# Optimization experiments

Measured on AMD Instinct MI355X. Metric: run time of the kernel, lower is better.

## Reference

```python
import jax, jax.numpy as jnp
import numpy as np

SELECTED_CLASSES = 5  # selected_classes init arg; loop body is identical each iteration
EPS = 1e-5            # nn.InstanceNorm2d default eps


def setup_inputs() -> dict:
    key = jax.random.key(0)
    k1, k2, k3 = jax.random.split(key, 3)
    x = jax.random.normal(k1, (8, 256, 128, 128), dtype=jnp.float32)
    masks = jax.random.uniform(k2, (8, 512, 512), dtype=jnp.float32)
    conv_w = jax.random.normal(k3, (1, 3, 7, 7), dtype=jnp.float32) * 0.05  # CFR_branches[0], no bias
    in_gamma = jnp.ones((256,), dtype=jnp.float32)   # InstanceNorm2d affine weight
    in_beta = jnp.zeros((256,), dtype=jnp.float32)   # InstanceNorm2d affine bias
    return {"x": x, "masks": masks, "conv_w": conv_w, "in_gamma": in_gamma, "in_beta": in_beta}


def reference(x, masks, conv_w, in_gamma, in_beta):
    B, C, H, W = x.shape
    m = masks[:, None, :, :] if masks.ndim == 3 else masks  # [B,1,Hm,Wm]
    # F.interpolate(..., size=(H,H), mode='bilinear', align_corners=False) -> half-pixel bilinear
    m = jax.image.resize(m, (B, 1, H, H), method="bilinear")
    mid = x * m                                             # [B,C,H,W]
    avg_out = jnp.mean(mid, axis=1, keepdims=True)          # [B,1,H,W]
    max_out = jnp.max(mid, axis=1, keepdims=True)           # [B,1,H,W]
    atten = jnp.concatenate([avg_out, max_out, m], axis=1)  # [B,3,H,W]
    atten = jax.lax.conv_general_dilated(
        atten, conv_w, window_strides=(1, 1), padding=[(3, 3), (3, 3)],
        dimension_numbers=("NCHW", "OIHW", "NCHW"))        # [B,1,H,W]
    atten = jax.nn.sigmoid(atten)
    out = mid * atten
    # set_class_mask_matrix: kmeans1d is not imported -> except branch -> all-ones mask;
    # Regional_Normalization therefore reduces to InstanceNorm2d(out).
    mu = jnp.mean(out, axis=(2, 3), keepdims=True)
    var = jnp.var(out, axis=(2, 3), keepdims=True)
    rn = (out - mu) * jax.lax.rsqrt(var + EPS)
    rn = rn * in_gamma[None, :, None, None] + in_beta[None, :, None, None]
    # loop over selected_classes produces identical outs (idx stays 0); sum == scale
    return jax.nn.relu(SELECTED_CLASSES * rn)
```

## Files before the change

### kernel.cpp

```cpp
#include <hip/hip_runtime.h>
#include <math.h>

#define BB 8
#define CC 256
#define HH 128
#define WW 128
#define HWP 16384
#define MH 512
#define MW 512
#define NPIX (BB*HWP)
#define IQ 4096

__global__ __launch_bounds__(256) void k1(const float* __restrict__ masks,
                                          const float* __restrict__ x,
                                          float* __restrict__ m_out,
                                          float* __restrict__ cs,
                                          float* __restrict__ cm) {
    int bid = blockIdx.x, tid = threadIdx.x;
    if ((bid & 1) == 0) {
        int t = (bid >> 1) * 256 + tid;
        int j = t & 127, i = (t >> 7) & 127, b = t >> 14;
        const float Wt[8] = {1.f, 3.f, 5.f, 7.f, 7.f, 5.f, 3.f, 1.f};
        const float* mb = masks + (size_t)b * (MH * MW);
        int r0 = 4 * i - 2, c0 = 4 * j - 2;
        float cwgt[8];
        int ccl[8];
        float sh = 0.f;
        #pragma unroll
        for (int q = 0; q < 8; q++) {
            int c = c0 + q;
            bool v = (unsigned)c < (unsigned)MW;
            cwgt[q] = v ? Wt[q] : 0.f;
            sh += cwgt[q];
            ccl[q] = min(max(c, 0), MW - 1);
        }
        float acc = 0.f, sv = 0.f;
        #pragma unroll
        for (int p = 0; p < 8; p++) {
            int r = r0 + p;
            bool v = (unsigned)r < (unsigned)MH;
            float wp = v ? Wt[p] : 0.f;
            sv += wp;
            const float* row = mb + (size_t)min(max(r, 0), MH - 1) * MW;
            float ra = 0.f;
            #pragma unroll
            for (int q = 0; q < 8; q++) ra += cwgt[q] * row[ccl[q]];
            acc += wp * ra;
        }
        m_out[t] = acc / (sv * sh);
    } else {
        int id = bid >> 1;
        int chunk = id & 15;
        int g = (id >> 4) & 3;
        int b = id >> 6;
        int qi = chunk * 256 + tid;
        const float4* xb = (const float4*)x + ((size_t)(b * CC + g * 64)) * IQ + qi;
        float4 s = {0.f, 0.f, 0.f, 0.f};
        float4 mx = {-INFINITY, -INFINITY, -INFINITY, -INFINITY};
        #pragma unroll 8
        for (int c = 0; c < 64; c++) {
            float4 v = xb[(size_t)c * IQ];
            s.x += v.x; s.y += v.y; s.z += v.z; s.w += v.w;
            mx.x = fmaxf(mx.x, v.x); mx.y = fmaxf(mx.y, v.y);
            mx.z = fmaxf(mx.z, v.z); mx.w = fmaxf(mx.w, v.w);
        }
        size_t o = (size_t)g * (NPIX / 4) + (size_t)b * IQ + qi;
        ((float4*)cs)[o] = s;
        ((float4*)cm)[o] = mx;
    }
}

#define TW 64
#define TH 4
#define IW 70
#define IH 10
#define PITCH 72
__global__ __launch_bounds__(256) void k2(const float* __restrict__ m,
                                          const float* __restrict__ cs,
                                          const float* __restrict__ cm,
                                          const float* __restrict__ cw,
                                          float* __restrict__ wprod) {
    __shared__ float w[147];
    __shared__ float pa[IH * PITCH], px[IH * PITCH], pm[IH * PITCH];
    int tid = threadIdx.x, bid = blockIdx.x;
    int bx = bid & 1, by = (bid >> 1) & 31, b = bid >> 6;
    if (tid < 147) w[tid] = cw[tid];
    int ox = bx * TW - 3, oy = by * TH - 3;
    for (int idx = tid; idx < IW * IH; idx += 256) {
        int r = idx / IW, c = idx - r * IW;
        int gi = oy + r, gj = ox + c;
        float av = 0.f, mxv = 0.f, mv = 0.f;
        if ((unsigned)gi < (unsigned)HH && (unsigned)gj < (unsigned)WW) {
            int p = b * HWP + gi * WW + gj;
            mv = m[p];
            float s = cs[p] + cs[p + NPIX] + cs[p + 2 * NPIX] + cs[p + 3 * NPIX];
            float mmx = fmaxf(fmaxf(cm[p], cm[p + NPIX]),
                              fmaxf(cm[p + 2 * NPIX], cm[p + 3 * NPIX]));
            av = mv * s * (1.f / 256.f);
            mxv = mv * mmx;
        }
        pa[r * PITCH + c] = av;
        px[r * PITCH + c] = mxv;
        pm[r * PITCH + c] = mv;
    }
    __syncthreads();
    int col = tid & 63, r = tid >> 6;
    float acc = 0.f;
    #pragma unroll
    for (int di = 0; di < 7; di++) {
        #pragma unroll
        for (int dj = 0; dj < 7; dj++) {
            int li = (r + di) * PITCH + col + dj;
            acc += w[di * 7 + dj] * pa[li];
            acc += w[49 + di * 7 + dj] * px[li];
            acc += w[98 + di * 7 + dj] * pm[li];
        }
    }
    float at = 1.f / (1.f + expf(-acc));
    float res = pm[(r + 3) * PITCH + col + 3] * at;
    wprod[b * HWP + (by * TH + r) * WW + bx * TW + col] = res;
}

__global__ __launch_bounds__(256) void k3(const float* __restrict__ x,
                                          const float* __restrict__ wprod,
                                          const float* __restrict__ gamma,
                                          const float* __restrict__ beta,
                                          float* __restrict__ out) {
    int bc = blockIdx.x;
    int b = bc >> 8, c = bc & 255;
    const float4* xp = (const float4*)(x + (size_t)bc * HWP);
    const float4* wp = (const float4*)(wprod + (size_t)b * HWP);
    float4 o[16];
    float s = 0.f, ss = 0.f;
    #pragma unroll
    for (int k = 0; k < 16; k++) {
        int idx = threadIdx.x + k * 256;
        float4 xv = xp[idx];
        float4 wv = wp[idx];
        float4 ov;
        ov.x = xv.x * wv.x; ov.y = xv.y * wv.y;
        ov.z = xv.z * wv.z; ov.w = xv.w * wv.w;
        o[k] = ov;
        s += ov.x + ov.y + ov.z + ov.w;
        ss += ov.x * ov.x + ov.y * ov.y + ov.z * ov.z + ov.w * ov.w;
    }
    #pragma unroll
    for (int off = 32; off; off >>= 1) {
        s += __shfl_down(s, off, 64);
        ss += __shfl_down(ss, off, 64);
    }
    __shared__ float ls[4], lss[4];
    __shared__ float smu, srs;
    int wave = threadIdx.x >> 6, lane = threadIdx.x & 63;
    if (lane == 0) { ls[wave] = s; lss[wave] = ss; }
    __syncthreads();
    if (threadIdx.x == 0) {
        float S = ls[0] + ls[1] + ls[2] + ls[3];
        float SS = lss[0] + lss[1] + lss[2] + lss[3];
        float mu = S * (1.f / HWP);
        float var = fmaxf(SS * (1.f / HWP) - mu * mu, 0.f);
        smu = mu;
        srs = rsqrtf(var + 1e-5f);
    }
    __syncthreads();
    float mu = smu;
    float g5 = 5.f * srs * gamma[c];
    float b5 = 5.f * beta[c];
    float4* op = (float4*)(out + (size_t)bc * HWP);
    #pragma unroll
    for (int k = 0; k < 16; k++) {
        int idx = threadIdx.x + k * 256;
        float4 ov = o[k], r;
        r.x = fmaxf(fmaf(ov.x - mu, g5, b5), 0.f);
        r.y = fmaxf(fmaf(ov.y - mu, g5, b5), 0.f);
        r.z = fmaxf(fmaf(ov.z - mu, g5, b5), 0.f);
        r.w = fmaxf(fmaf(ov.w - mu, g5, b5), 0.f);
        op[idx] = r;
    }
}

extern "C" void kernel_launch(void* const* d_in, const int* in_sizes, int n_in,
                              void* d_out, int out_size, void* d_ws, size_t ws_size,
                              hipStream_t stream) {
    const float* x      = (const float*)d_in[0];
    const float* masks  = (const float*)d_in[1];
    const float* conv_w = (const float*)d_in[2];
    const float* gamma  = (const float*)d_in[3];
    const float* beta   = (const float*)d_in[4];
    float* out = (float*)d_out;

    float* ws = (float*)d_ws;
    float* m_arr = ws;
    float* cs    = ws + (size_t)NPIX;
    float* cm    = ws + (size_t)5 * NPIX;
    float* wprod = ws + (size_t)9 * NPIX;

    k1<<<1024, 256, 0, stream>>>(masks, x, m_arr, cs, cm);
    k2<<<512, 256, 0, stream>>>(m_arr, cs, cm, conv_w, wprod);
    k3<<<BB * CC, 256, 0, stream>>>(x, wprod, gamma, beta, out);
}
```

Baseline: 266.4 us.

## Fuse three kernels into one persistent kernel with atomic-counter grid barriers

Merges the mask/channel-reduction, attention-conv, and instance-norm kernels into one launch of 1024 blocks. Stages are separated by global atomic counters with spin-waits instead of kernel boundaries. The norm stage no longer holds outputs in registers; it re-reads x and wprod in a second pass, and each block handles two channels. This removes launch gaps and register pressure but adds a memset, spin-wait barriers that need all 1024 blocks co-resident, and an extra read of x.

```diff
diff --git a/kernel.cpp b/kernel.cpp
--- a/kernel.cpp
+++ b/kernel.cpp
@@ -11,20 +11,56 @@
 #define NPIX (BB*HWP)
 #define IQ 4096
 
-__global__ __launch_bounds__(256) void k1(const float* __restrict__ masks,
-                                          const float* __restrict__ x,
-                                          float* __restrict__ m_out,
-                                          float* __restrict__ cs,
-                                          float* __restrict__ cm) {
-    int bid = blockIdx.x, tid = threadIdx.x;
-    if ((bid & 1) == 0) {
-        int t = (bid >> 1) * 256 + tid;
+#define TW 64
+#define TH 4
+#define IW 70
+#define IH 10
+#define PITCH 72
+
+__device__ __forceinline__ void publish(unsigned* ctr) {
+    __syncthreads();
+    if (threadIdx.x == 0)
+        __hip_atomic_fetch_add(ctr, 1u, __ATOMIC_RELEASE, __HIP_MEMORY_SCOPE_AGENT);
+}
+
+__device__ __forceinline__ void waitc(unsigned* ctr, unsigned tgt) {
+    if (threadIdx.x == 0) {
+        while (__hip_atomic_load(ctr, __ATOMIC_ACQUIRE, __HIP_MEMORY_SCOPE_AGENT) < tgt)
+            __builtin_amdgcn_s_sleep(16);
+    }
+    __syncthreads();
+}
+
+__global__ __launch_bounds__(256, 4) void fused(const float* __restrict__ masks,
+                                                const float* __restrict__ x,
+                                                const float* __restrict__ cw,
+                                                const float* __restrict__ gamma,
+                                                const float* __restrict__ beta,
+                                                float* __restrict__ out,
+                                                unsigned* __restrict__ ctrs,
+                                                float* __restrict__ wsb) {
+    float* m_arr = wsb;
+    float* cs    = wsb + (size_t)NPIX;
+    float* cm    = wsb + (size_t)5 * NPIX;
+    float* wprod = wsb + (size_t)9 * NPIX;
+    unsigned* ctr0 = ctrs;
+    unsigned* ctr1 = ctrs + 32;
+
+    __shared__ float w[147];
+    __shared__ float pa[IH * PITCH], px[IH * PITCH], pm[IH * PITCH];
+    __shared__ float ls[4], lss[4], smu, srs;
+
+    const int bid = blockIdx.x, tid = threadIdx.x;
+    const bool even = (bid & 1) == 0;
+    const int e = bid >> 1;
+
+    if (even) {
+        int t = e * 256 + tid;
         int j = t & 127, i = (t >> 7) & 127, b = t >> 14;
         const float Wt[8] = {1.f, 3.f, 5.f, 7.f, 7.f, 5.f, 3.f, 1.f};
         const float* mb = masks + (size_t)b * (MH * MW);
         int r0 = 4 * i - 2, c0 = 4 * j - 2;
-        float cwgt[8];
-        int ccl[8];
+        float cwgt[8]; int ccl[8];
         float sh = 0.f;
         #pragma unroll
         for (int q = 0; q < 8; q++) {
@@ -47,12 +83,9 @@
             for (int q = 0; q < 8; q++) ra += cwgt[q] * row[ccl[q]];
             acc += wp * ra;
         }
-        m_out[t] = acc / (sv * sh);
+        m_arr[t] = acc / (sv * sh);
     } else {
-        int id = bid >> 1;
-        int chunk = id & 15;
-        int g = (id >> 4) & 3;
-        int b = id >> 6;
+        int chunk = e & 15, g = (e >> 4) & 3, b = e >> 6;
         int qi = chunk * 256 + tid;
         const float4* xb = (const float4*)x + ((size_t)(b * CC + g * 64)) * IQ + qi;
         float4 s = {0.f, 0.f, 0.f, 0.f};
@@ -68,114 +101,101 @@
         ((float4*)cs)[o] = s;
         ((float4*)cm)[o] = mx;
     }
-}
-
-#define TW 64
-#define TH 4
-#define IW 70
-#define IH 10
-#define PITCH 72
-__global__ __launch_bounds__(256) void k2(const float* __restrict__ m,
-                                          const float* __restrict__ cs,
-                                          const float* __restrict__ cm,
-                                          const float* __restrict__ cw,
-                                          float* __restrict__ wprod) {
-    __shared__ float w[147];
-    __shared__ float pa[IH * PITCH], px[IH * PITCH], pm[IH * PITCH];
-    int tid = threadIdx.x, bid = blockIdx.x;
-    int bx = bid & 1, by = (bid >> 1) & 31, b = bid >> 6;
-    if (tid < 147) w[tid] = cw[tid];
-    int ox = bx * TW - 3, oy = by * TH - 3;
-    for (int idx = tid; idx < IW * IH; idx += 256) {
-        int r = idx / IW, c = idx - r * IW;
-        int gi = oy + r, gj = ox + c;
-        float av = 0.f, mxv = 0.f, mv = 0.f;
-        if ((unsigned)gi < (unsigned)HH && (unsigned)gj < (unsigned)WW) {
-            int p = b * HWP + gi * WW + gj;
-            mv = m[p];
-            float s = cs[p] + cs[p + NPIX] + cs[p + 2 * NPIX] + cs[p + 3 * NPIX];
-            float mmx = fmaxf(fmaxf(cm[p], cm[p + NPIX]),
-                              fmaxf(cm[p + 2 * NPIX], cm[p + 3 * NPIX]));
-            av = mv * s * (1.f / 256.f);
-            mxv = mv * mmx;
-        }
-        pa[r * PITCH + c] = av;
-        px[r * PITCH + c] = mxv;
-        pm[r * PITCH + c] = mv;
-    }
-    __syncthreads();
-    int col = tid & 63, r = tid >> 6;
-    float acc = 0.f;
+    publish(ctr0);
+
+    if (even) {
+        waitc(ctr0, 1024);
+        int bx = e & 1, by = (e >> 1) & 31, b = e >> 6;
+        if (tid < 147) w[tid] = cw[tid];
+        int ox = bx * TW - 3, oy = by * TH - 3;
+        for (int idx = tid; idx < IW * IH; idx += 256) {
+            int r = idx / IW, c = idx - r * IW;
+            int gi = oy + r, gj = ox + c;
+            float av = 0.f, mxv = 0.f, mv = 0.f;
+            if ((unsigned)gi < (unsigned)HH && (unsigned)gj < (unsigned)WW) {
+                int p = b * HWP + gi * WW + gj;
+                mv = m_arr[p];
+                float s = cs[p] + cs[p + NPIX] + cs[p + 2 * NPIX] + cs[p + 3 * NPIX];
+                float mmx = fmaxf(fmaxf(cm[p], cm[p + NPIX]),
+                                  fmaxf(cm[p + 2 * NPIX], cm[p + 3 * NPIX]));
+                av = mv * s * (1.f / 256.f);
+                mxv = mv * mmx;
+            }
+            pa[r * PITCH + c] = av;
+            px[r * PITCH + c] = mxv;
+            pm[r * PITCH + c] = mv;
+        }
+        __syncthreads();
+        int col = tid & 63, r = tid >> 6;
+        float acc = 0.f;
+        #pragma unroll
+        for (int di = 0; di < 7; di++) {
+            #pragma unroll
+            for (int dj = 0; dj < 7; dj++) {
+                int li = (r + di) * PITCH + col + dj;
+                acc += w[di * 7 + dj] * pa[li];
+                acc += w[49 + di * 7 + dj] * px[li];
+                acc += w[98 + di * 7 + dj] * pm[li];
+            }
+        }
+        float at = 1.f / (1.f + expf(-acc));
+        float res = pm[(r + 3) * PITCH + col + 3] * at;
+        wprod[b * HWP + (by * TH + r) * WW + bx * TW + col] = res;
+        publish(ctr1);
+    }
+
+    waitc(ctr1, 512);
     #pragma unroll
-    for (int di = 0; di < 7; di++) {
-        #pragma unroll
-        for (int dj = 0; dj < 7; dj++) {
-            int li = (r + di) * PITCH + col + dj;
-            acc += w[di * 7 + dj] * pa[li];
-            acc += w[49 + di * 7 + dj] * px[li];
-            acc += w[98 + di * 7 + dj] * pm[li];
-        }
-    }
-    float at = 1.f / (1.f + expf(-acc));
-    float res = pm[(r + 3) * PITCH + col + 3] * at;
-    wprod[b * HWP + (by * TH + r) * WW + bx * TW + col] = res;
-}
-
-__global__ __launch_bounds__(256) void k3(const float* __restrict__ x,
-                                          const float* __restrict__ wprod,
-                                          const float* __restrict__ gamma,
-                                          const float* __restrict__ beta,
-                                          float* __restrict__ out) {
-    int bc = blockIdx.x;
-    int b = bc >> 8, c = bc & 255;
-    const float4* xp = (const float4*)(x + (size_t)bc * HWP);
-    const float4* wp = (const float4*)(wprod + (size_t)b * HWP);
-    float4 o[16];
-    float s = 0.f, ss = 0.f;
-    #pragma unroll
-    for (int k = 0; k < 16; k++) {
-        int idx = threadIdx.x + k * 256;
-        float4 xv = xp[idx];
-        float4 wv = wp[idx];
-        float4 ov;
-        ov.x = xv.x * wv.x; ov.y = xv.y * wv.y;
-        ov.z = xv.z * wv.z; ov.w = xv.w * wv.w;
-        o[k] = ov;
-        s += ov.x + ov.y + ov.z + ov.w;
-        ss += ov.x * ov.x + ov.y * ov.y + ov.z * ov.z + ov.w * ov.w;
-    }
-    #pragma unroll
-    for (int off = 32; off; off >>= 1) {
-        s += __shfl_down(s, off, 64);
-        ss += __shfl_down(ss, off, 64);
-    }
-    __shared__ float ls[4], lss[4];
-    __shared__ float smu, srs;
-    int wave = threadIdx.x >> 6, lane = threadIdx.x & 63;
-    if (lane == 0) { ls[wave] = s; lss[wave] = ss; }
-    __syncthreads();
-    if (threadIdx.x == 0) {
-        float S = ls[0] + ls[1] + ls[2] + ls[3];
-        float SS = lss[0] + lss[1] + lss[2] + lss[3];
-        float mu = S * (1.f / HWP);
-        float var = fmaxf(SS * (1.f / HWP) - mu * mu, 0.f);
-        smu = mu;
-        srs = rsqrtf(var + 1e-5f);
-    }
-    __syncthreads();
-    float mu = smu;
-    float g5 = 5.f * srs * gamma[c];
-    float b5 = 5.f * beta[c];
-    float4* op = (float4*)(out + (size_t)bc * HWP);
-    #pragma unroll
-    for (int k = 0; k < 16; k++) {
-        int idx = threadIdx.x + k * 256;
-        float4 ov = o[k], r;
-        r.x = fmaxf(fmaf(ov.x - mu, g5, b5), 0.f);
-        r.y = fmaxf(fmaf(ov.y - mu, g5, b5), 0.f);
-        r.z = fmaxf(fmaf(ov.z - mu, g5, b5), 0.f);
-        r.w = fmaxf(fmaf(ov.w - mu, g5, b5), 0.f);
-        op[idx] = r;
+    for (int pl = 0; pl < 2; pl++) {
+        int bc = bid + pl * 1024;
+        int b = bc >> 8, c = bc & 255;
+        const float4* xp = (const float4*)(x + (size_t)bc * HWP);
+        const float4* wp = (const float4*)(wprod + (size_t)b * HWP);
+        float s = 0.f, ss = 0.f;
+        #pragma unroll 4
+        for (int k = 0; k < 16; k++) {
+            int idx = tid + k * 256;
+            float4 xv = xp[idx];
+            float4 wv = wp[idx];
+            float a0 = xv.x * wv.x, a1 = xv.y * wv.y;
+            float a2 = xv.z * wv.z, a3 = xv.w * wv.w;
+            s += a0 + a1 + a2 + a3;
+            ss += a0 * a0 + a1 * a1 + a2 * a2 + a3 * a3;
+        }
+        #pragma unroll
+        for (int off = 32; off; off >>= 1) {
+            s += __shfl_down(s, off, 64);
+            ss += __shfl_down(ss, off, 64);
+        }
+        int wave = tid >> 6, lane = tid & 63;
+        if (pl) __syncthreads();
+        if (lane == 0) { ls[wave] = s; lss[wave] = ss; }
+        __syncthreads();
+        if (tid == 0) {
+            float S = ls[0] + ls[1] + ls[2] + ls[3];
+            float SS = lss[0] + lss[1] + lss[2] + lss[3];
+            float mu = S * (1.f / HWP);
+            float var = fmaxf(SS * (1.f / HWP) - mu * mu, 0.f);
+            smu = mu;
+            srs = rsqrtf(var + 1e-5f);
+        }
+        __syncthreads();
+        float mu = smu;
+        float g5 = 5.f * srs * gamma[c];
+        float b5 = 5.f * beta[c];
+        float4* op = (float4*)(out + (size_t)bc * HWP);
+        #pragma unroll 4
+        for (int k = 0; k < 16; k++) {
+            int idx = tid + k * 256;
+            float4 xv = xp[idx];
+            float4 wv = wp[idx];
+            float4 r;
+            r.x = fmaxf(fmaf(xv.x * wv.x - mu, g5, b5), 0.f);
+            r.y = fmaxf(fmaf(xv.y * wv.y - mu, g5, b5), 0.f);
+            r.z = fmaxf(fmaf(xv.z * wv.z - mu, g5, b5), 0.f);
+            r.w = fmaxf(fmaf(xv.w * wv.w - mu, g5, b5), 0.f);
+            op[idx] = r;
+        }
     }
 }
 
@@ -189,13 +209,9 @@
     const float* beta   = (const float*)d_in[4];
     float* out = (float*)d_out;
 
-    float* ws = (float*)d_ws;
-    float* m_arr = ws;
-    float* cs    = ws + (size_t)NPIX;
-    float* cm    = ws + (size_t)5 * NPIX;
-    float* wprod = ws + (size_t)9 * NPIX;
-
-    k1<<<1024, 256, 0, stream>>>(masks, x, m_arr, cs, cm);
-    k2<<<512, 256, 0, stream>>>(m_arr, cs, cm, conv_w, wprod);
-    k3<<<BB * CC, 256, 0, stream>>>(x, wprod, gamma, beta, out);
-}
+    unsigned* ctrs = (unsigned*)d_ws;
+    float* wsb = (float*)d_ws + 128;
+
+    hipMemsetAsync(d_ws, 0, 512, stream);
+    fused<<<1024, 256, 0, stream>>>(masks, x, conv_w, gamma, beta, out, ctrs, wsb);
+}
```

New measurement: 445.1 us. 1.67x slower.
